# Kernel optimization log

Hardware: AMD Instinct MI355X
Metric: run time of the kernel (lower is better)

Reference implementation:

```python
import jax, jax.numpy as jnp
import numpy as np
import math

D = 8192      # data_dim = num simplices
B = 8         # batch
E = 131072    # Laplacian nnz (avg degree 16)
HID = 256     # hidden_dim
TDIM = 128    # time_embed_dim


def setup_inputs() -> dict:
    key = jax.random.key(0)
    ks = jax.random.split(key, 16)

    def lin(k, i, o):
        return jax.random.normal(k, (i, o), jnp.float32) / np.sqrt(i).astype(np.float32)

    return {
        "x": jax.random.normal(ks[0], (B, D), jnp.float32),
        "t": jax.random.uniform(ks[1], (B,), jnp.float32),
        "ld_idx": jax.random.randint(ks[2], (2, E), 0, D),
        "ld_val": jax.random.normal(ks[3], (E,), jnp.float32) * 0.1,
        "lu_idx": jax.random.randint(ks[4], (2, E), 0, D),
        "lu_val": jax.random.normal(ks[5], (E,), jnp.float32) * 0.1,
        "W1": jax.random.normal(ks[6], (1, HID, 3), jnp.float32),        # SNN layer1 weight [in, out, 1+down+up]
        "W2": jax.random.normal(ks[7], (HID, 1, 3), jnp.float32) / np.sqrt(HID).astype(np.float32),
        "t_w1": lin(ks[8], TDIM, HID), "t_b1": jnp.zeros((HID,), jnp.float32),
        "t_w2": lin(ks[9], HID, HID), "t_b2": jnp.zeros((HID,), jnp.float32),
        "map_w": lin(ks[10], D, HID), "map_b": jnp.zeros((HID,), jnp.float32),
        "o_w1": lin(ks[11], HID, HID), "o_b1": jnp.zeros((HID,), jnp.float32),
        "o_w2": lin(ks[12], HID, D), "o_b2": jnp.zeros((D,), jnp.float32),
    }


def timestep_embedding(t, dim, max_period=10000):
    half = dim // 2  # dim=128 is even, no zero padding column
    freqs = jnp.exp(-math.log(max_period) * jnp.arange(half, dtype=t.dtype) / half)
    args = t[:, None] * freqs[None, :]
    return jnp.concatenate([jnp.cos(args), jnp.sin(args)], axis=-1)


def spmm(idx, val, x):
    # sparse [N,N] @ dense [N,C] via COO gather + segment-sum scatter
    return jax.ops.segment_sum(val[:, None] * x[idx[1]], idx[0], num_segments=x.shape[0])


def snn_layer(x, W, ld_idx, ld_val, lu_idx, lu_val):
    # conv_order_down = conv_order_up = 1 -> terms: [identity, L_down x, L_up x]
    terms = jnp.stack([x, spmm(ld_idx, ld_val, x), spmm(lu_idx, lu_val, x)], axis=2)  # [N, Cin, 3]
    return jnp.einsum('nik,iok->no', terms, W)


def reference(x, t, ld_idx, ld_val, lu_idx, lu_val, W1, W2,
              t_w1, t_b1, t_w2, t_b2, map_w, map_b, o_w1, o_b1, o_w2, o_b2):
    # time embedding MLP
    t_emb = timestep_embedding(t, TDIM)                    # [B, TDIM]
    t_out = jax.nn.silu(t_emb @ t_w1 + t_b1) @ t_w2 + t_b2  # [B, HID]

    # SNN (2 layers): layer1 update_func=None -> raw y; layer2 update_func='id' -> raw y
    def snn(xi):  # xi: [N]
        h = snn_layer(xi[:, None], W1, ld_idx, ld_val, lu_idx, lu_val)  # [N, HID]
        y = snn_layer(h, W2, ld_idx, ld_val, lu_idx, lu_val)            # [N, 1]
        return y[:, 0]

    x_out = jax.vmap(snn)(x)                               # [B, N]

    # ResNet_FC with 0 res blocks -> just the map Linear
    h = x_out @ map_w + map_b                              # [B, HID]

    out = jax.nn.silu((h + t_out) @ o_w1 + o_b1) @ o_w2 + o_b2  # [B, D]
    return out
```

## Files before the change

### kernel.cpp

```cpp
#include <hip/hip_runtime.h>
#include <math.h>

#define D 8192
#define B 8
#define E 131072
#define HID 256
#define TDIM 128

#define OFF_XT 0
#define OFF_DD 65536
#define OFF_UU 131072
#define OFF_HB 196608
#define OFF_HC 262144
#define OFF_Y  327680
#define OFF_G  393216
#define OFF_S  395264
#define OFF_SC 397312

__global__ __launch_bounds__(1024) void k_front(
        const float* __restrict__ x, const float* __restrict__ t,
        const float* __restrict__ W1, const float* __restrict__ W2,
        const float* __restrict__ t_w1, const float* __restrict__ t_b1,
        const float* __restrict__ t_w2, const float* __restrict__ t_b2,
        const float* __restrict__ map_b, const float* __restrict__ o_b2,
        float* __restrict__ ws, float* __restrict__ out)
{
    const int blk = blockIdx.x, tid = threadIdx.x;
    if (blk < 64) {
        int idx = blk * 1024 + tid;
        int b = idx & 7, n = idx >> 3;
        ws[OFF_XT + idx] = x[b * D + n];
        ws[OFF_DD + idx] = 0.f;
        ws[OFF_UU + idx] = 0.f;
        out[idx] = o_b2[idx & (D - 1)];
        return;
    }
    if (blk < 72) {
        const int b = blk - 64;
        __shared__ float emb[TDIM];
        __shared__ float h1[HID];
        __shared__ float part[4][HID];
        float tb = t[b];
        if (tid < TDIM) {
            int j = tid & 63;
            float freq = expf(-0.14391156831212787f * (float)j);
            float a = tb * freq;
            emb[tid] = (tid < 64) ? cosf(a) : sinf(a);
        }
        __syncthreads();
        const int j = tid & 255, ic = tid >> 8;
        float z = 0.f;
        #pragma unroll 8
        for (int i = ic * 32; i < ic * 32 + 32; i++) z += emb[i] * t_w1[i * HID + j];
        part[ic][j] = z;
        __syncthreads();
        if (tid < HID) {
            float zz = t_b1[tid] + part[0][tid] + part[1][tid] + part[2][tid] + part[3][tid];
            h1[tid] = zz / (1.f + expf(-zz));
        }
        __syncthreads();
        float z2 = 0.f;
        #pragma unroll 8
        for (int i = ic * 64; i < ic * 64 + 64; i++) z2 += h1[i] * t_w2[i * HID + j];
        part[ic][j] = z2;
        __syncthreads();
        if (tid < HID) {
            float zz = t_b2[tid] + part[0][tid] + part[1][tid] + part[2][tid] + part[3][tid];
            (ws + OFF_G)[b * HID + tid] = map_b[tid] + zz;
        }
        return;
    }
    {
        int w = tid >> 6, lane = tid & 63;
        if (w < 9) {
            int jj = w / 3, k = w % 3;
            float acc = 0.f;
            #pragma unroll
            for (int q = 0; q < 4; q++) {
                int i = lane + 64 * q;
                acc += W1[i * 3 + k] * W2[i * 3 + jj];
            }
            #pragma unroll
            for (int off = 32; off > 0; off >>= 1) acc += __shfl_down(acc, off, 64);
            if (lane == 0) (ws + OFF_SC)[jj * 3 + k] = acc;
        }
    }
}

__global__ void k_scatter(const int* __restrict__ ldi, const float* __restrict__ ldv,
                          const int* __restrict__ lui, const float* __restrict__ luv,
                          const float* __restrict__ src_d, const float* __restrict__ src_u,
                          float* __restrict__ dst_d, float* __restrict__ dst_u)
{
    int gtid = blockIdx.x * 256 + threadIdx.x;
    int b = gtid & 7;
    int e = gtid >> 3;
    const int* idx; const float* val; const float* src; float* dst;
    if (e < E) { idx = ldi; val = ldv; src = src_d; dst = dst_d; }
    else       { e -= E; idx = lui; val = luv; src = src_u; dst = dst_u; }
    int row = idx[e];
    int col = idx[E + e];
    float v = val[e];
    atomicAdd(&dst[row * 8 + b], v * src[col * 8 + b]);
}

__global__ void k_mid(float* __restrict__ ws)
{
    int idx = blockIdx.x * 256 + threadIdx.x;
    const float* sc = ws + OFF_SC;
    float xv = ws[OFF_XT + idx];
    float dv = ws[OFF_DD + idx];
    float uv = ws[OFF_UU + idx];
    ws[OFF_Y  + idx] = sc[0] * xv + sc[1] * dv + sc[2] * uv;
    ws[OFF_HB + idx] = sc[3] * xv + sc[4] * dv + sc[5] * uv;
    ws[OFF_HC + idx] = sc[6] * xv + sc[7] * dv + sc[8] * uv;
}

__global__ void k_map(const float* __restrict__ map_w, float* __restrict__ ws)
{
    __shared__ float ysl[128 * 8];
    int blk = blockIdx.x, tid = threadIdx.x;
    const float* y = ws + OFF_Y;
    float* g = ws + OFF_G;
    int base = blk * 128 * 8;
    for (int i = tid; i < 1024; i += 256) ysl[i] = y[base + i];
    __syncthreads();
    float acc[8] = {0.f, 0.f, 0.f, 0.f, 0.f, 0.f, 0.f, 0.f};
    int nbase = blk * 128;
    for (int r = 0; r < 128; r++) {
        float w = map_w[(nbase + r) * HID + tid];
        #pragma unroll
        for (int b = 0; b < 8; b++) acc[b] += ysl[r * 8 + b] * w;
    }
    #pragma unroll
    for (int b = 0; b < 8; b++) atomicAdd(&g[b * HID + tid], acc[b]);
}

__global__ void k_mlp(const float* __restrict__ o_w1, const float* __restrict__ o_b1,
                      float* __restrict__ ws)
{
    __shared__ float gs[HID];
    int b = blockIdx.x, tid = threadIdx.x;
    const float* g = ws + OFF_G;
    float* s = ws + OFF_S;
    gs[tid] = g[b * HID + tid];
    __syncthreads();
    float z = o_b1[tid];
    #pragma unroll 4
    for (int i = 0; i < HID; i++) z += gs[i] * o_w1[i * HID + tid];
    s[b * HID + tid] = z / (1.f + expf(-z));
}

__global__ void k_out(const float* __restrict__ o_w2, const float* __restrict__ ws,
                      float* __restrict__ out)
{
    __shared__ float ssl[8 * 64];
    int nc = blockIdx.x, jc = blockIdx.y, tid = threadIdx.x;
    const float* s = ws + OFF_S;
    for (int i = tid; i < 512; i += 256) {
        int b = i >> 6, jj = i & 63;
        ssl[i] = s[b * HID + jc * 64 + jj];
    }
    __syncthreads();
    int n = nc * 256 + tid;
    float acc[8] = {0.f, 0.f, 0.f, 0.f, 0.f, 0.f, 0.f, 0.f};
    for (int jj = 0; jj < 64; jj++) {
        int j = jc * 64 + jj;
        float w = o_w2[j * D + n];
        #pragma unroll
        for (int b = 0; b < 8; b++) acc[b] += ssl[b * 64 + jj] * w;
    }
    #pragma unroll
    for (int b = 0; b < 8; b++) atomicAdd(&out[b * D + n], acc[b]);
}

extern "C" void kernel_launch(void* const* d_in, const int* in_sizes, int n_in,
                              void* d_out, int out_size, void* d_ws, size_t ws_size,
                              hipStream_t stream)
{
    const float* x     = (const float*)d_in[0];
    const float* t     = (const float*)d_in[1];
    const int*   ldi   = (const int*)  d_in[2];
    const float* ldv   = (const float*)d_in[3];
    const int*   lui   = (const int*)  d_in[4];
    const float* luv   = (const float*)d_in[5];
    const float* W1    = (const float*)d_in[6];
    const float* W2    = (const float*)d_in[7];
    const float* t_w1  = (const float*)d_in[8];
    const float* t_b1  = (const float*)d_in[9];
    const float* t_w2  = (const float*)d_in[10];
    const float* t_b2  = (const float*)d_in[11];
    const float* map_w = (const float*)d_in[12];
    const float* map_b = (const float*)d_in[13];
    const float* o_w1  = (const float*)d_in[14];
    const float* o_b1  = (const float*)d_in[15];
    const float* o_w2  = (const float*)d_in[16];
    const float* o_b2  = (const float*)d_in[17];
    float* out = (float*)d_out;
    float* ws  = (float*)d_ws;

    float* xT = ws + OFF_XT;
    float* dd = ws + OFF_DD;
    float* uu = ws + OFF_UU;
    float* hb = ws + OFF_HB;
    float* hc = ws + OFF_HC;
    float* y  = ws + OFF_Y;

    k_front<<<73, 1024, 0, stream>>>(x, t, W1, W2, t_w1, t_b1, t_w2, t_b2,
                                     map_b, o_b2, ws, out);
    k_scatter<<<2 * E * 8 / 256, 256, 0, stream>>>(ldi, ldv, lui, luv, xT, xT, dd, uu);
    k_mid<<<256, 256, 0, stream>>>(ws);
    k_scatter<<<2 * E * 8 / 256, 256, 0, stream>>>(ldi, ldv, lui, luv, hb, hc, y, y);
    k_map<<<64, 256, 0, stream>>>(map_w, ws);
    k_mlp<<<8, 256, 0, stream>>>(o_w1, o_b1, ws);
    k_out<<<dim3(32, 4), 256, 0, stream>>>(o_w2, ws, out);
}
```

Measured before the change: 72.75 us.

## Fuse mid combine into second scatter and map, widen map and MLP parallelism

```diff
diff --git a/kernel.cpp b/kernel.cpp
--- a/kernel.cpp
+++ b/kernel.cpp
@@ -10,12 +10,10 @@
 #define OFF_XT 0
 #define OFF_DD 65536
 #define OFF_UU 131072
-#define OFF_HB 196608
-#define OFF_HC 262144
-#define OFF_Y  327680
-#define OFF_G  393216
-#define OFF_S  395264
-#define OFF_SC 397312
+#define OFF_Y  196608
+#define OFF_G  262144
+#define OFF_S  264192
+#define OFF_SC 266240
 
 __global__ __launch_bounds__(1024) void k_front(
         const float* __restrict__ x, const float* __restrict__ t,
@@ -32,6 +30,7 @@
         ws[OFF_XT + idx] = x[b * D + n];
         ws[OFF_DD + idx] = 0.f;
         ws[OFF_UU + idx] = 0.f;
+        ws[OFF_Y  + idx] = 0.f;
         out[idx] = o_b2[idx & (D - 1)];
         return;
     }
@@ -87,68 +86,86 @@
     }
 }
 
-__global__ void k_scatter(const int* __restrict__ ldi, const float* __restrict__ ldv,
-                          const int* __restrict__ lui, const float* __restrict__ luv,
-                          const float* __restrict__ src_d, const float* __restrict__ src_u,
-                          float* __restrict__ dst_d, float* __restrict__ dst_u)
+__global__ void k_scat1(const int* __restrict__ ldi, const float* __restrict__ ldv,
+                        const int* __restrict__ lui, const float* __restrict__ luv,
+                        float* __restrict__ ws)
 {
     int gtid = blockIdx.x * 256 + threadIdx.x;
     int b = gtid & 7;
     int e = gtid >> 3;
-    const int* idx; const float* val; const float* src; float* dst;
-    if (e < E) { idx = ldi; val = ldv; src = src_d; dst = dst_d; }
-    else       { e -= E; idx = lui; val = luv; src = src_u; dst = dst_u; }
+    const int* idx; const float* val; float* dst;
+    if (e < E) { idx = ldi; val = ldv; dst = ws + OFF_DD; }
+    else       { e -= E; idx = lui; val = luv; dst = ws + OFF_UU; }
     int row = idx[e];
     int col = idx[E + e];
     float v = val[e];
-    atomicAdd(&dst[row * 8 + b], v * src[col * 8 + b]);
-}
-
-__global__ void k_mid(float* __restrict__ ws)
-{
-    int idx = blockIdx.x * 256 + threadIdx.x;
+    atomicAdd(&dst[row * 8 + b], v * ws[OFF_XT + col * 8 + b]);
+}
+
+__global__ void k_scat2(const int* __restrict__ ldi, const float* __restrict__ ldv,
+                        const int* __restrict__ lui, const float* __restrict__ luv,
+                        float* __restrict__ ws)
+{
+    int gtid = blockIdx.x * 256 + threadIdx.x;
+    int b = gtid & 7;
+    int e = gtid >> 3;
     const float* sc = ws + OFF_SC;
-    float xv = ws[OFF_XT + idx];
-    float dv = ws[OFF_DD + idx];
-    float uv = ws[OFF_UU + idx];
-    ws[OFF_Y  + idx] = sc[0] * xv + sc[1] * dv + sc[2] * uv;
-    ws[OFF_HB + idx] = sc[3] * xv + sc[4] * dv + sc[5] * uv;
-    ws[OFF_HC + idx] = sc[6] * xv + sc[7] * dv + sc[8] * uv;
+    const int* idx; const float* val; float c0, c1, c2;
+    if (e < E) { idx = ldi; val = ldv; c0 = sc[3]; c1 = sc[4]; c2 = sc[5]; }
+    else       { e -= E; idx = lui; val = luv; c0 = sc[6]; c1 = sc[7]; c2 = sc[8]; }
+    int row = idx[e];
+    int col = idx[E + e];
+    float v = val[e];
+    int ci = col * 8 + b;
+    float h = c0 * ws[OFF_XT + ci] + c1 * ws[OFF_DD + ci] + c2 * ws[OFF_UU + ci];
+    atomicAdd(&ws[OFF_Y + row * 8 + b], v * h);
 }
 
 __global__ void k_map(const float* __restrict__ map_w, float* __restrict__ ws)
 {
-    __shared__ float ysl[128 * 8];
+    __shared__ float yf[32 * 8];
     int blk = blockIdx.x, tid = threadIdx.x;
-    const float* y = ws + OFF_Y;
+    const float* sc = ws + OFF_SC;
     float* g = ws + OFF_G;
-    int base = blk * 128 * 8;
-    for (int i = tid; i < 1024; i += 256) ysl[i] = y[base + i];
+    int base = blk * 32 * 8;
+    {
+        float a0 = sc[0], a1 = sc[1], a2 = sc[2];
+        int i = base + tid;
+        yf[tid] = a0 * ws[OFF_XT + i] + a1 * ws[OFF_DD + i] + a2 * ws[OFF_UU + i]
+                + ws[OFF_Y + i];
+    }
     __syncthreads();
     float acc[8] = {0.f, 0.f, 0.f, 0.f, 0.f, 0.f, 0.f, 0.f};
-    int nbase = blk * 128;
-    for (int r = 0; r < 128; r++) {
+    int nbase = blk * 32;
+    #pragma unroll 4
+    for (int r = 0; r < 32; r++) {
         float w = map_w[(nbase + r) * HID + tid];
         #pragma unroll
-        for (int b = 0; b < 8; b++) acc[b] += ysl[r * 8 + b] * w;
+        for (int b = 0; b < 8; b++) acc[b] += yf[r * 8 + b] * w;
     }
     #pragma unroll
     for (int b = 0; b < 8; b++) atomicAdd(&g[b * HID + tid], acc[b]);
 }
 
-__global__ void k_mlp(const float* __restrict__ o_w1, const float* __restrict__ o_b1,
-                      float* __restrict__ ws)
+__global__ __launch_bounds__(1024) void k_mlp(const float* __restrict__ o_w1,
+                                              const float* __restrict__ o_b1,
+                                              float* __restrict__ ws)
 {
     __shared__ float gs[HID];
+    __shared__ float part[4][HID];
     int b = blockIdx.x, tid = threadIdx.x;
-    const float* g = ws + OFF_G;
-    float* s = ws + OFF_S;
-    gs[tid] = g[b * HID + tid];
-    __syncthreads();
-    float z = o_b1[tid];
-    #pragma unroll 4
-    for (int i = 0; i < HID; i++) z += gs[i] * o_w1[i * HID + tid];
-    s[b * HID + tid] = z / (1.f + expf(-z));
+    if (tid < HID) gs[tid] = (ws + OFF_G)[b * HID + tid];
+    __syncthreads();
+    int j = tid & 255, ic = tid >> 8;
+    float z = 0.f;
+    #pragma unroll 8
+    for (int i = ic * 64; i < ic * 64 + 64; i++) z += gs[i] * o_w1[i * HID + j];
+    part[ic][j] = z;
+    __syncthreads();
+    if (tid < HID) {
+        float zz = o_b1[tid] + part[0][tid] + part[1][tid] + part[2][tid] + part[3][tid];
+        (ws + OFF_S)[b * HID + tid] = zz / (1.f + expf(-zz));
+    }
 }
 
 __global__ void k_out(const float* __restrict__ o_w2, const float* __restrict__ ws,
@@ -164,6 +181,7 @@
     __syncthreads();
     int n = nc * 256 + tid;
     float acc[8] = {0.f, 0.f, 0.f, 0.f, 0.f, 0.f, 0.f, 0.f};
+    #pragma unroll 4
     for (int jj = 0; jj < 64; jj++) {
         int j = jc * 64 + jj;
         float w = o_w2[j * D + n];
@@ -199,19 +217,11 @@
     float* out = (float*)d_out;
     float* ws  = (float*)d_ws;
 
-    float* xT = ws + OFF_XT;
-    float* dd = ws + OFF_DD;
-    float* uu = ws + OFF_UU;
-    float* hb = ws + OFF_HB;
-    float* hc = ws + OFF_HC;
-    float* y  = ws + OFF_Y;
-
     k_front<<<73, 1024, 0, stream>>>(x, t, W1, W2, t_w1, t_b1, t_w2, t_b2,
                                      map_b, o_b2, ws, out);
-    k_scatter<<<2 * E * 8 / 256, 256, 0, stream>>>(ldi, ldv, lui, luv, xT, xT, dd, uu);
-    k_mid<<<256, 256, 0, stream>>>(ws);
-    k_scatter<<<2 * E * 8 / 256, 256, 0, stream>>>(ldi, ldv, lui, luv, hb, hc, y, y);
-    k_map<<<64, 256, 0, stream>>>(map_w, ws);
-    k_mlp<<<8, 256, 0, stream>>>(o_w1, o_b1, ws);
+    k_scat1<<<2 * E * 8 / 256, 256, 0, stream>>>(ldi, ldv, lui, luv, ws);
+    k_scat2<<<2 * E * 8 / 256, 256, 0, stream>>>(ldi, ldv, lui, luv, ws);
+    k_map<<<256, 256, 0, stream>>>(map_w, ws);
+    k_mlp<<<8, 1024, 0, stream>>>(o_w1, o_b1, ws);
     k_out<<<dim3(32, 4), 256, 0, stream>>>(o_w2, ws, out);
 }
```

Result: faster. 62.78 us (-13.7%).

## Replace atomic COO scatter with bucketed row gather SpMV and fuse MLP into output

Applied to the files above, without the earlier changes.

```diff
diff --git a/kernel.cpp b/kernel.cpp
--- a/kernel.cpp
+++ b/kernel.cpp
@@ -6,33 +6,30 @@
 #define E 131072
 #define HID 256
 #define TDIM 128
+#define MAXDEG 64
 
 #define OFF_XT 0
 #define OFF_DD 65536
 #define OFF_UU 131072
-#define OFF_HB 196608
-#define OFF_HC 262144
-#define OFF_Y  327680
-#define OFF_G  393216
-#define OFF_S  395264
-#define OFF_SC 397312
+#define OFF_Y0 196608
+#define OFF_Y1 262144
+#define OFF_G  327680
+#define OFF_SC 329728
+#define IOFF_CNT  329760
+#define IOFF_EDGE 346144
 
 __global__ __launch_bounds__(1024) void k_front(
         const float* __restrict__ x, const float* __restrict__ t,
         const float* __restrict__ W1, const float* __restrict__ W2,
         const float* __restrict__ t_w1, const float* __restrict__ t_b1,
         const float* __restrict__ t_w2, const float* __restrict__ t_b2,
-        const float* __restrict__ map_b, const float* __restrict__ o_b2,
-        float* __restrict__ ws, float* __restrict__ out)
+        const float* __restrict__ map_b, float* __restrict__ ws)
 {
     const int blk = blockIdx.x, tid = threadIdx.x;
     if (blk < 64) {
         int idx = blk * 1024 + tid;
-        int b = idx & 7, n = idx >> 3;
-        ws[OFF_XT + idx] = x[b * D + n];
-        ws[OFF_DD + idx] = 0.f;
-        ws[OFF_UU + idx] = 0.f;
-        out[idx] = o_b2[idx & (D - 1)];
+        ws[OFF_XT + idx] = x[(idx & 7) * D + (idx >> 3)];
+        if (idx < 16384) ((int*)ws)[IOFF_CNT + idx] = 0;
         return;
     }
     if (blk < 72) {
@@ -87,91 +84,132 @@
     }
 }
 
-__global__ void k_scatter(const int* __restrict__ ldi, const float* __restrict__ ldv,
-                          const int* __restrict__ lui, const float* __restrict__ luv,
-                          const float* __restrict__ src_d, const float* __restrict__ src_u,
-                          float* __restrict__ dst_d, float* __restrict__ dst_u)
-{
-    int gtid = blockIdx.x * 256 + threadIdx.x;
-    int b = gtid & 7;
-    int e = gtid >> 3;
-    const int* idx; const float* val; const float* src; float* dst;
-    if (e < E) { idx = ldi; val = ldv; src = src_d; dst = dst_d; }
-    else       { e -= E; idx = lui; val = luv; src = src_u; dst = dst_u; }
+__global__ void k_fill(const int* __restrict__ ldi, const float* __restrict__ ldv,
+                       const int* __restrict__ lui, const float* __restrict__ luv,
+                       float* __restrict__ ws)
+{
+    int t = blockIdx.x * 256 + threadIdx.x;
+    int m = t >> 17;
+    int e = t & (E - 1);
+    const int* idx = m ? lui : ldi;
+    const float* val = m ? luv : ldv;
     int row = idx[e];
     int col = idx[E + e];
     float v = val[e];
-    atomicAdd(&dst[row * 8 + b], v * src[col * 8 + b]);
-}
-
-__global__ void k_mid(float* __restrict__ ws)
-{
-    int idx = blockIdx.x * 256 + threadIdx.x;
+    int bucket = m * D + row;
+    int* cnt = (int*)ws + IOFF_CNT;
+    int2* edges = (int2*)((int*)ws + IOFF_EDGE);
+    int slot = atomicAdd(&cnt[bucket], 1);
+    edges[bucket * MAXDEG + slot] = make_int2(col, __float_as_int(v));
+}
+
+__global__ void k_spmv1(float* __restrict__ ws)
+{
+    int t = blockIdx.x * 256 + threadIdx.x;
+    int m = t >> 16, r = (t >> 3) & (D - 1), b = t & 7;
+    int bucket = m * D + r;
+    const int* cnt = (const int*)ws + IOFF_CNT;
+    const int2* edges = (const int2*)((const int*)ws + IOFF_EDGE);
+    int deg = cnt[bucket];
+    const int2* ep = edges + bucket * MAXDEG;
+    float acc = 0.f;
+    #pragma unroll 2
+    for (int p = 0; p < deg; p++) {
+        int2 ed = ep[p];
+        acc += __int_as_float(ed.y) * ws[OFF_XT + ed.x * 8 + b];
+    }
+    ws[(m ? OFF_UU : OFF_DD) + r * 8 + b] = acc;
+}
+
+__global__ void k_spmv2(float* __restrict__ ws)
+{
+    int t = blockIdx.x * 256 + threadIdx.x;
+    int m = t >> 16, r = (t >> 3) & (D - 1), b = t & 7;
+    int bucket = m * D + r;
     const float* sc = ws + OFF_SC;
-    float xv = ws[OFF_XT + idx];
-    float dv = ws[OFF_DD + idx];
-    float uv = ws[OFF_UU + idx];
-    ws[OFF_Y  + idx] = sc[0] * xv + sc[1] * dv + sc[2] * uv;
-    ws[OFF_HB + idx] = sc[3] * xv + sc[4] * dv + sc[5] * uv;
-    ws[OFF_HC + idx] = sc[6] * xv + sc[7] * dv + sc[8] * uv;
+    const int* cnt = (const int*)ws + IOFF_CNT;
+    const int2* edges = (const int2*)((const int*)ws + IOFF_EDGE);
+    int deg = cnt[bucket];
+    const int2* ep = edges + bucket * MAXDEG;
+    float c0, c1, c2;
+    if (m == 0) { c0 = sc[3]; c1 = sc[4]; c2 = sc[5]; }
+    else        { c0 = sc[6]; c1 = sc[7]; c2 = sc[8]; }
+    float acc = 0.f;
+    #pragma unroll 2
+    for (int p = 0; p < deg; p++) {
+        int2 ed = ep[p];
+        int ci = ed.x * 8 + b;
+        float h = c0 * ws[OFF_XT + ci] + c1 * ws[OFF_DD + ci] + c2 * ws[OFF_UU + ci];
+        acc += __int_as_float(ed.y) * h;
+    }
+    int i = r * 8 + b;
+    if (m == 0) {
+        acc += sc[0] * ws[OFF_XT + i] + sc[1] * ws[OFF_DD + i] + sc[2] * ws[OFF_UU + i];
+        ws[OFF_Y0 + i] = acc;
+    } else {
+        ws[OFF_Y1 + i] = acc;
+    }
 }
 
 __global__ void k_map(const float* __restrict__ map_w, float* __restrict__ ws)
 {
-    __shared__ float ysl[128 * 8];
+    __shared__ float yl[128 * 8];
     int blk = blockIdx.x, tid = threadIdx.x;
-    const float* y = ws + OFF_Y;
     float* g = ws + OFF_G;
     int base = blk * 128 * 8;
-    for (int i = tid; i < 1024; i += 256) ysl[i] = y[base + i];
+    for (int i = tid; i < 1024; i += 256)
+        yl[i] = ws[OFF_Y0 + base + i] + ws[OFF_Y1 + base + i];
     __syncthreads();
     float acc[8] = {0.f, 0.f, 0.f, 0.f, 0.f, 0.f, 0.f, 0.f};
     int nbase = blk * 128;
+    #pragma unroll 4
     for (int r = 0; r < 128; r++) {
         float w = map_w[(nbase + r) * HID + tid];
         #pragma unroll
-        for (int b = 0; b < 8; b++) acc[b] += ysl[r * 8 + b] * w;
+        for (int b = 0; b < 8; b++) acc[b] += yl[r * 8 + b] * w;
     }
     #pragma unroll
     for (int b = 0; b < 8; b++) atomicAdd(&g[b * HID + tid], acc[b]);
 }
 
-__global__ void k_mlp(const float* __restrict__ o_w1, const float* __restrict__ o_b1,
-                      float* __restrict__ ws)
-{
-    __shared__ float gs[HID];
-    int b = blockIdx.x, tid = threadIdx.x;
+__global__ void k_out(const float* __restrict__ o_w1, const float* __restrict__ o_b1,
+                      const float* __restrict__ o_w2, const float* __restrict__ o_b2,
+                      const float* __restrict__ ws, float* __restrict__ out)
+{
+    __shared__ float gs[B * HID];
+    __shared__ float ssl[B * HID];
+    int blk = blockIdx.x, tid = threadIdx.x;
     const float* g = ws + OFF_G;
-    float* s = ws + OFF_S;
-    gs[tid] = g[b * HID + tid];
+    for (int i = tid; i < B * HID; i += 256) gs[i] = g[i];
     __syncthreads();
-    float z = o_b1[tid];
+    {
+        float z[8];
+        float bias = o_b1[tid];
+        #pragma unroll
+        for (int b = 0; b < 8; b++) z[b] = bias;
+        for (int i = 0; i < HID; i++) {
+            float w = o_w1[i * HID + tid];
+            #pragma unroll
+            for (int b = 0; b < 8; b++) z[b] += gs[b * HID + i] * w;
+        }
+        #pragma unroll
+        for (int b = 0; b < 8; b++)
+            ssl[b * HID + tid] = z[b] / (1.f + expf(-z[b]));
+    }
+    __syncthreads();
+    int n = blk * 256 + tid;
+    float acc[8];
+    float bias2 = o_b2[n];
+    #pragma unroll
+    for (int b = 0; b < 8; b++) acc[b] = bias2;
     #pragma unroll 4
-    for (int i = 0; i < HID; i++) z += gs[i] * o_w1[i * HID + tid];
-    s[b * HID + tid] = z / (1.f + expf(-z));
-}
-
-__global__ void k_out(const float* __restrict__ o_w2, const float* __restrict__ ws,
-                      float* __restrict__ out)
-{
-    __shared__ float ssl[8 * 64];
-    int nc = blockIdx.x, jc = blockIdx.y, tid = threadIdx.x;
-    const float* s = ws + OFF_S;
-    for (int i = tid; i < 512; i += 256) {
-        int b = i >> 6, jj = i & 63;
-        ssl[i] = s[b * HID + jc * 64 + jj];
-    }
-    __syncthreads();
-    int n = nc * 256 + tid;
-    float acc[8] = {0.f, 0.f, 0.f, 0.f, 0.f, 0.f, 0.f, 0.f};
-    for (int jj = 0; jj < 64; jj++) {
-        int j = jc * 64 + jj;
+    for (int j = 0; j < HID; j++) {
         float w = o_w2[j * D + n];
         #pragma unroll
-        for (int b = 0; b < 8; b++) acc[b] += ssl[b * 64 + jj] * w;
+        for (int b = 0; b < 8; b++) acc[b] += ssl[b * HID + j] * w;
     }
     #pragma unroll
-    for (int b = 0; b < 8; b++) atomicAdd(&out[b * D + n], acc[b]);
+    for (int b = 0; b < 8; b++) out[b * D + n] = acc[b];
 }
 
 extern "C" void kernel_launch(void* const* d_in, const int* in_sizes, int n_in,
@@ -199,19 +237,10 @@
     float* out = (float*)d_out;
     float* ws  = (float*)d_ws;
 
-    float* xT = ws + OFF_XT;
-    float* dd = ws + OFF_DD;
-    float* uu = ws + OFF_UU;
-    float* hb = ws + OFF_HB;
-    float* hc = ws + OFF_HC;
-    float* y  = ws + OFF_Y;
-
-    k_front<<<73, 1024, 0, stream>>>(x, t, W1, W2, t_w1, t_b1, t_w2, t_b2,
-                                     map_b, o_b2, ws, out);
-    k_scatter<<<2 * E * 8 / 256, 256, 0, stream>>>(ldi, ldv, lui, luv, xT, xT, dd, uu);
-    k_mid<<<256, 256, 0, stream>>>(ws);
-    k_scatter<<<2 * E * 8 / 256, 256, 0, stream>>>(ldi, ldv, lui, luv, hb, hc, y, y);
+    k_front<<<73, 1024, 0, stream>>>(x, t, W1, W2, t_w1, t_b1, t_w2, t_b2, map_b, ws);
+    k_fill<<<2 * E / 256, 256, 0, stream>>>(ldi, ldv, lui, luv, ws);
+    k_spmv1<<<512, 256, 0, stream>>>(ws);
+    k_spmv2<<<512, 256, 0, stream>>>(ws);
     k_map<<<64, 256, 0, stream>>>(map_w, ws);
-    k_mlp<<<8, 256, 0, stream>>>(o_w1, o_b1, ws);
-    k_out<<<dim3(32, 4), 256, 0, stream>>>(o_w2, ws, out);
-}
+    k_out<<<32, 256, 0, stream>>>(o_w1, o_b1, o_w2, o_b2, ws, out);
+}
```

Result: slower. 94.64 us (+30.1%).
